# Kernel optimization log

Hardware: AMD Instinct MI355X
Metric: run time of the kernel (lower is better)

The kernel has to match this reference:

```python
import jax, jax.numpy as jnp
import numpy as np

N_HEAD = 16
N_EMBD = 1024
SCALE = 1.0 / np.sqrt(N_EMBD // N_HEAD)
NEG_INF = -1e9


def setup_inputs() -> dict:
    key = jax.random.key(0)
    ks = jax.random.split(key, 9)
    B, T, C = 4, 2048, N_EMBD
    std = 1.0 / np.sqrt(C)
    x = jax.random.normal(ks[0], (B, T, C), dtype=jnp.float32)
    attention_mask = jnp.ones((B, T), dtype=jnp.int32)
    Wq = jax.random.normal(ks[1], (C, C), dtype=jnp.float32) * std
    Wk = jax.random.normal(ks[2], (C, C), dtype=jnp.float32) * std
    Wv = jax.random.normal(ks[3], (C, C), dtype=jnp.float32) * std
    Wp = jax.random.normal(ks[4], (C, C), dtype=jnp.float32) * std
    bq = jax.random.normal(ks[5], (C,), dtype=jnp.float32) * 0.01
    bk = jax.random.normal(ks[6], (C,), dtype=jnp.float32) * 0.01
    bv = jax.random.normal(ks[7], (C,), dtype=jnp.float32) * 0.01
    bp = jax.random.normal(ks[8], (C,), dtype=jnp.float32) * 0.01
    return {"x": x, "attention_mask": attention_mask,
            "Wq": Wq, "bq": bq, "Wk": Wk, "bk": bk,
            "Wv": Wv, "bv": bv, "Wp": Wp, "bp": bp}


def reference(x, attention_mask, Wq, bq, Wk, bk, Wv, bv, Wp, bp):
    B, T, C = x.shape
    H, D = N_HEAD, C // N_HEAD
    # projections -> [B, H, T, D]
    def split_heads(y):
        return y.reshape(B, T, H, D).transpose(0, 2, 1, 3)
    q = split_heads(x @ Wq + bq)
    k = split_heads(x @ Wk + bk)
    v = split_heads(x @ Wv + bv)
    # scores [B, H, T, T]
    att = jnp.einsum('bhqd,bhkd->bhqk', q, k) * SCALE
    causal = jnp.tril(jnp.ones((T, T), dtype=bool))
    att = jnp.where(causal[None, None], att, NEG_INF)
    pad = attention_mask[:, None, None, :] != 0  # [B,1,1,T]
    att = jnp.where(pad, att, NEG_INF)
    att = jax.nn.softmax(att, axis=-1)
    # dropout p=0.0 (eval) -> identity
    y = jnp.einsum('bhqk,bhkd->bhqd', att, v)
    y = y.transpose(0, 2, 1, 3).reshape(B, T, C)
    return y @ Wp + bp
```

## Files before the change

### kernel.cpp

```cpp
#include <hip/hip_runtime.h>

typedef unsigned short u16;
typedef unsigned int u32;
typedef unsigned long long u64;
typedef __bf16 bf16x8 __attribute__((ext_vector_type(8)));
typedef unsigned short u16x8 __attribute__((ext_vector_type(8)));
typedef unsigned short u16x4 __attribute__((ext_vector_type(4)));
typedef unsigned int u32x4 __attribute__((ext_vector_type(4)));
typedef float f32x4 __attribute__((ext_vector_type(4)));

#define B_  4
#define T_  2048
#define C_  1024
#define H_  16
#define D_  64

__device__ __forceinline__ u16 f2b(float f) {
  unsigned u = __builtin_bit_cast(unsigned, f);
  return (u16)((u + 0x8000u) >> 16);
}
__device__ __forceinline__ bf16x8 bcast8(u16x8 v) { return __builtin_bit_cast(bf16x8, v); }

__device__ __forceinline__ void gl_lds16(const void* g, void* l) {
  __builtin_amdgcn_global_load_lds((const __attribute__((address_space(1))) u32*)g,
                                   (__attribute__((address_space(3))) u32*)l, 16, 0, 0);
}

__global__ __launch_bounds__(256) void xconv_kernel(const float* __restrict__ x, u16* __restrict__ xb) {
  const size_t i = ((size_t)blockIdx.x * 256 + threadIdx.x) * 8;
  const float4 a = *reinterpret_cast<const float4*>(x + i);
  const float4 b = *reinterpret_cast<const float4*>(x + i + 4);
  u16x8 h;
  h[0] = f2b(a.x); h[1] = f2b(a.y); h[2] = f2b(a.z); h[3] = f2b(a.w);
  h[4] = f2b(b.x); h[5] = f2b(b.y); h[6] = f2b(b.z); h[7] = f2b(b.w);
  *reinterpret_cast<u16x8*>(xb + i) = h;
}

__global__ void wconv_kernel(const float* __restrict__ Wq, const float* __restrict__ Wk,
                             const float* __restrict__ Wv, const float* __restrict__ Wp,
                             u16* __restrict__ wt) {
  __shared__ float tile[32][33];
  const int z = blockIdx.z;
  const float* W = (z == 0) ? Wq : (z == 1) ? Wk : (z == 2) ? Wv : Wp;
  u16* out = wt + (size_t)z * C_ * C_;
  const int n0 = blockIdx.x * 32, k0 = blockIdx.y * 32;
  const int tx = threadIdx.x, ty = threadIdx.y;
  #pragma unroll
  for (int i = 0; i < 4; ++i)
    tile[ty + i * 8][tx] = W[(size_t)(k0 + ty + i * 8) * C_ + n0 + tx];
  __syncthreads();
  #pragma unroll
  for (int i = 0; i < 4; ++i)
    out[(size_t)(n0 + ty + i * 8) * C_ + k0 + tx] = f2b(tile[tx][ty + i * 8]);
}

#define GSTAGE(ldsbase, gsrc) do {                                                   \
    _Pragma("unroll")                                                                \
    for (int i_ = 0; i_ < 4; ++i_) {                                                 \
      const int off_ = wid * 1024 + i_ * 4096;                                       \
      const int row_ = (off_ >> 7) + (lane >> 3);                                    \
      const int cs_  = ((lane & 7) ^ ((lane >> 3) & 7)) * 16;                        \
      gl_lds16((const char*)(gsrc) + (size_t)row_ * 2048 + cs_,                      \
               (char*)(ldsbase) + off_);                                             \
    }                                                                                \
  } while (0)

__global__ __launch_bounds__(256) void qkv_gemm(const u16* __restrict__ xb,
    const u16* __restrict__ wt, const float* __restrict__ bq,
    const float* __restrict__ bk, const float* __restrict__ bv,
    u16* __restrict__ qkv) {
  __shared__ __attribute__((aligned(16))) u16 As[2][128][64];
  __shared__ __attribute__((aligned(16))) u16 Bs[2][128][64];
  const int id = blockIdx.x;
  const int xcd = id & 7, cc = id >> 3;
  const int bm = xcd * 8 + (cc / 24);
  const int bnt = cc % 24;
  const int tid = threadIdx.x;
  const int lane = tid & 63, wid = tid >> 6;
  const int wr = wid >> 1, wc = wid & 1;
  const int m0 = bm * 128, n0 = bnt * 128;

  f32x4 acc[4][4] = {};

  const char* abase = (const char*)xb + (size_t)m0 * 2048;
  const char* bbase = (const char*)wt + (size_t)n0 * 2048;

  const int ph0 = (((lane >> 4)) ^ (lane & 7)) << 3;
  const int ph1 = ((4 + (lane >> 4)) ^ (lane & 7)) << 3;

  GSTAGE(&As[0][0][0], abase);
  GSTAGE(&Bs[0][0][0], bbase);
  __syncthreads();

  for (int t = 0; t < 16; ++t) {
    const int cur = t & 1;
    if (t + 1 < 16) {
      GSTAGE(&As[cur ^ 1][0][0], abase + (t + 1) * 128);
      GSTAGE(&Bs[cur ^ 1][0][0], bbase + (t + 1) * 128);
    }
    bf16x8 af[2][4], bf[2][4];
    #pragma unroll
    for (int r = 0; r < 4; ++r) {
      const int row = wr * 64 + r * 16 + (lane & 15);
      af[0][r] = bcast8(*reinterpret_cast<const u16x8*>(&As[cur][row][ph0]));
      af[1][r] = bcast8(*reinterpret_cast<const u16x8*>(&As[cur][row][ph1]));
    }
    #pragma unroll
    for (int c = 0; c < 4; ++c) {
      const int row = wc * 64 + c * 16 + (lane & 15);
      bf[0][c] = bcast8(*reinterpret_cast<const u16x8*>(&Bs[cur][row][ph0]));
      bf[1][c] = bcast8(*reinterpret_cast<const u16x8*>(&Bs[cur][row][ph1]));
    }
    #pragma unroll
    for (int kk = 0; kk < 2; ++kk)
      #pragma unroll
      for (int r = 0; r < 4; ++r)
        #pragma unroll
        for (int c = 0; c < 4; ++c)
          acc[r][c] = __builtin_amdgcn_mfma_f32_16x16x32_bf16(af[kk][r], bf[kk][c], acc[r][c], 0, 0, 0);
    __syncthreads();
  }
  const int which = n0 >> 10;
  const float* bias = (which == 0) ? bq : (which == 1) ? bk : bv;
  #pragma unroll
  for (int r = 0; r < 4; ++r) {
    #pragma unroll
    for (int c = 0; c < 4; ++c) {
      const int col = n0 + wc * 64 + c * 16 + (lane & 15);
      const int cold = col & 1023;
      const float bv_ = bias[cold];
      const int h = cold >> 6, d = cold & 63;
      #pragma unroll
      for (int p = 0; p < 4; ++p) {
        const int row = m0 + wr * 64 + r * 16 + (lane >> 4) * 4 + p;
        const int bb = row >> 11, t = row & (T_ - 1);
        int dd = d;
        if (which == 1) dd = (d & 7) | ((((d >> 3) ^ (t & 7)) & 7) << 3);
        qkv[(((size_t)which * 64 + bb * H_ + h) * T_ + t) * D_ + dd] = f2b(acc[r][c][p] + bv_);
      }
    }
  }
}

__global__ __launch_bounds__(256) void vtrans_kernel(const u16* __restrict__ qkv, u16* __restrict__ vt) {
  __shared__ u16 tile[64][64];
  const int bh = blockIdx.y;
  const int t0 = blockIdx.x * 64;
  const u16* V = qkv + (size_t)(128 + bh) * (T_ * D_);
  const int tid = threadIdx.x;
  #pragma unroll
  for (int i = 0; i < 2; ++i) {
    const int tl = (tid >> 3) + i * 32;
    const int d0 = (tid & 7) * 8;
    const u16x8 v = *reinterpret_cast<const u16x8*>(&V[(size_t)(t0 + tl) * D_ + d0]);
    const int swz = (d0 >> 3) << 3;
    #pragma unroll
    for (int j = 0; j < 8; ++j)
      tile[d0 + j][tl ^ swz] = v[j];
  }
  __syncthreads();
  #pragma unroll
  for (int i = 0; i < 2; ++i) {
    const int d = (tid >> 3) + i * 32;
    const int c0 = (tid & 7) * 8;
    const u16x8 w = *reinterpret_cast<const u16x8*>(&tile[d][c0 ^ ((d >> 3) << 3)]);
    const int cc = (((c0 >> 3) ^ (d & 7)) << 3);
    *reinterpret_cast<u16x8*>(&vt[((size_t)bh * D_ + d) * T_ + t0 + cc]) = w;
  }
}

__global__ __launch_bounds__(256) void attn_kernel(const u16* __restrict__ qkv,
    const u16* __restrict__ vt, u16* __restrict__ yb) {
  __shared__ __attribute__((aligned(16))) u16 Ks[2][64][64];
  __shared__ __attribute__((aligned(16))) u16 Vs[2][64][64];
  const int bid = blockIdx.x;
  const int wgid = (bid & 7) * 64 + (bid >> 3);
  const int bh = wgid >> 3, pj = wgid & 7;
  const int tid = threadIdx.x, lane = tid & 63, wid = tid >> 6;
  const int g = lane >> 4;
  const u16* Q  = qkv + (size_t)bh * (T_ * D_);
  const u16* K  = qkv + (size_t)(64 + bh) * (T_ * D_);
  const u16* Vt = vt + (size_t)bh * (D_ * T_);
  const int b_ = bh >> 4, h_ = bh & 15;

  const int sw_off = wid * 2048;
  const int vrow0  = wid * 16 + (lane >> 3);
  const int vcol   = (lane & 7) * 16;

  #pragma unroll 1
  for (int seg = 0; seg < 2; ++seg) {
    const int qt = (seg == 0) ? pj : 15 - pj;
    const int q0 = qt * 128;
    const int nt = 2 * qt + 2;
    const int q0w = q0 + wid * 32;

    bf16x8 qf[2][2];
    #pragma unroll
    for (int r = 0; r < 2; ++r)
      #pragma unroll
      for (int ks = 0; ks < 2; ++ks)
        qf[r][ks] = bcast8(*reinterpret_cast<const u16x8*>(
            &Q[(size_t)(q0 + wid * 32 + r * 16 + (lane & 15)) * D_ + ks * 32 + g * 8]));

    f32x4 o[2][4] = {};
    float l_r[2] = {};

#define STAGE(bufi, tt) do {                                                        \
      const char* ksrc_ = (const char*)(K + (size_t)(tt) * 64 * D_);                \
      const char* vsrc_ = (const char*)(Vt + (size_t)(tt) * 64);                    \
      _Pragma("unroll")                                                             \
      for (int i_ = 0; i_ < 2; ++i_) {                                              \
        const int off_ = sw_off + i_ * 1024;                                        \
        gl_lds16(ksrc_ + off_ + lane * 16, (char*)&Ks[bufi][0][0] + off_);          \
        gl_lds16(vsrc_ + (size_t)(vrow0 + i_ * 8) * (T_ * 2) + vcol,                \
                 (char*)&Vs[bufi][0][0] + off_);                                    \
      }                                                                             \
    } while (0)

    STAGE(0, 0);
    __syncthreads();

    for (int t = 0; t < nt; ++t) {
      const int cur = t & 1;
      if (t + 1 < nt) STAGE((t + 1) & 1, t + 1);
      const int kv0 = t * 64;
      if (kv0 <= q0w + 31) {
        f32x4 s[2][4] = {};
        #pragma unroll
        for (int c = 0; c < 4; ++c) {
          const int krow = c * 16 + (lane & 15);
          const bf16x8 kf0 = bcast8(*reinterpret_cast<const u16x8*>(
              &Ks[cur][krow][(g ^ (krow & 7)) << 3]));
          const bf16x8 kf1 = bcast8(*reinterpret_cast<const u16x8*>(
              &Ks[cur][krow][((g + 4) ^ (krow & 7)) << 3]));
          #pragma unroll
          for (int r = 0; r < 2; ++r) {
            s[r][c] = __builtin_amdgcn_mfma_f32_16x16x32_bf16(kf0, qf[r][0], s[r][c], 0, 0, 0);
            s[r][c] = __builtin_amdgcn_mfma_f32_16x16x32_bf16(kf1, qf[r][1], s[r][c], 0, 0, 0);
          }
        }
        bf16x8 vf[2][4];
        #pragma unroll
        for (int ks = 0; ks < 2; ++ks)
          #pragma unroll
          for (int c = 0; c < 4; ++c) {
            const int drow = c * 16 + (lane & 15);
            const char* rowp = (const char*)&Vs[cur][drow][0];
            const int sb0 = (((4 * ks + (g >> 1)) ^ (drow & 7)) << 4) + (g & 1) * 8;
            const int sb1 = (((4 * ks + 2 + (g >> 1)) ^ (drow & 7)) << 4) + (g & 1) * 8;
            const u64 lo = *reinterpret_cast<const u64*>(rowp + sb0);
            const u64 hi = *reinterpret_cast<const u64*>(rowp + sb1);
            u32x4 vw; vw[0] = (u32)lo; vw[1] = (u32)(lo >> 32); vw[2] = (u32)hi; vw[3] = (u32)(hi >> 32);
            vf[ks][c] = __builtin_bit_cast(bf16x8, vw);
          }
        u32x4 paw[2][2];
#define SMAX(MASKED) do {                                                           \
          _Pragma("unroll")                                                         \
          for (int r = 0; r < 2; ++r) {                                             \
            const int qpos = q0w + r * 16 + (lane & 15);                            \
            _Pragma("unroll")                                                       \
            for (int c = 0; c < 4; ++c) {                                           \
              const int kb = kv0 + c * 16 + g * 4;                                  \
              float e[4];                                                           \
              _Pragma("unroll")                                                     \
              for (int p = 0; p < 4; ++p) {                                         \
                e[p] = exp2f(fmaf(s[r][c][p], 0.1803368801111244f,                  \
                                  -17.312340444387028f));                           \
                if (MASKED) e[p] = (kb + p <= qpos) ? e[p] : 0.0f;                  \
                l_r[r] += e[p];                                                     \
              }                                                                     \
              u32 w0, w1;                                                           \
              asm("v_cvt_pk_bf16_f32 %0, %1, %2" : "=v"(w0) : "v"(e[0]), "v"(e[1]));\
              asm("v_cvt_pk_bf16_f32 %0, %1, %2" : "=v"(w1) : "v"(e[2]), "v"(e[3]));\
              paw[r][c >> 1][(c & 1) * 2] = w0;                                     \
              paw[r][c >> 1][(c & 1) * 2 + 1] = w1;                                 \
            }                                                                       \
          }                                                                         \
        } while (0)
        if (kv0 + 63 <= q0w) SMAX(false); else SMAX(true);
#undef SMAX
        #pragma unroll
        for (int ks = 0; ks < 2; ++ks)
          #pragma unroll
          for (int r = 0; r < 2; ++r) {
            const bf16x8 pa = __builtin_bit_cast(bf16x8, paw[r][ks]);
            #pragma unroll
            for (int c = 0; c < 4; ++c)
              o[r][c] = __builtin_amdgcn_mfma_f32_16x16x32_bf16(pa, vf[ks][c], o[r][c], 0, 0, 0);
          }
      }
      __syncthreads();
    }
#undef STAGE

    #pragma unroll
    for (int r = 0; r < 2; ++r) {
      float l = l_r[r];
      l += __shfl_xor(l, 16);
      l += __shfl_xor(l, 32);
      float linv[4];
      #pragma unroll
      for (int p = 0; p < 4; ++p)
        linv[p] = 1.0f / __shfl(l, g * 4 + p, 64);
      #pragma unroll
      for (int c = 0; c < 4; ++c) {
        const int d = c * 16 + (lane & 15);
        #pragma unroll
        for (int p = 0; p < 4; ++p) {
          const int qrow = q0w + r * 16 + g * 4 + p;
          yb[(size_t)(b_ * T_ + qrow) * C_ + h_ * D_ + d] = f2b(o[r][c][p] * linv[p]);
        }
      }
    }
  }
}

__global__ __launch_bounds__(256) void proj_gemm(const u16* __restrict__ yb,
    const u16* __restrict__ Bt, const float* __restrict__ bias, float* __restrict__ out) {
  __shared__ __attribute__((aligned(16))) u16 As[2][128][64];
  __shared__ __attribute__((aligned(16))) u16 Bs[2][128][64];
  const int id = blockIdx.x;
  const int xcd = id & 7, cc = id >> 3;
  const int bm = xcd * 8 + (cc / 8);
  const int bn = cc % 8;
  const int tid = threadIdx.x;
  const int lane = tid & 63, wid = tid >> 6;
  const int wr = wid >> 1, wc = wid & 1;
  const int m0 = bm * 128, n0 = bn * 128;

  f32x4 acc[4][4] = {};

  const char* abase = (const char*)yb + (size_t)m0 * 2048;
  const char* bbase = (const char*)Bt + (size_t)n0 * 2048;

  const int ph0 = (((lane >> 4)) ^ (lane & 7)) << 3;
  const int ph1 = ((4 + (lane >> 4)) ^ (lane & 7)) << 3;

  GSTAGE(&As[0][0][0], abase);
  GSTAGE(&Bs[0][0][0], bbase);
  __syncthreads();

  for (int t = 0; t < 16; ++t) {
    const int cur = t & 1;
    if (t + 1 < 16) {
      GSTAGE(&As[cur ^ 1][0][0], abase + (t + 1) * 128);
      GSTAGE(&Bs[cur ^ 1][0][0], bbase + (t + 1) * 128);
    }
    bf16x8 af[2][4], bf[2][4];
    #pragma unroll
    for (int r = 0; r < 4; ++r) {
      const int row = wr * 64 + r * 16 + (lane & 15);
      af[0][r] = bcast8(*reinterpret_cast<const u16x8*>(&As[cur][row][ph0]));
      af[1][r] = bcast8(*reinterpret_cast<const u16x8*>(&As[cur][row][ph1]));
    }
    #pragma unroll
    for (int c = 0; c < 4; ++c) {
      const int row = wc * 64 + c * 16 + (lane & 15);
      bf[0][c] = bcast8(*reinterpret_cast<const u16x8*>(&Bs[cur][row][ph0]));
      bf[1][c] = bcast8(*reinterpret_cast<const u16x8*>(&Bs[cur][row][ph1]));
    }
    #pragma unroll
    for (int kk = 0; kk < 2; ++kk)
      #pragma unroll
      for (int r = 0; r < 4; ++r)
        #pragma unroll
        for (int c = 0; c < 4; ++c)
          acc[r][c] = __builtin_amdgcn_mfma_f32_16x16x32_bf16(af[kk][r], bf[kk][c], acc[r][c], 0, 0, 0);
    __syncthreads();
  }
  #pragma unroll
  for (int r = 0; r < 4; ++r)
    #pragma unroll
    for (int c = 0; c < 4; ++c) {
      const int col = n0 + wc * 64 + c * 16 + (lane & 15);
      const float bv_ = bias[col];
      #pragma unroll
      for (int p = 0; p < 4; ++p) {
        const int row = m0 + wr * 64 + r * 16 + (lane >> 4) * 4 + p;
        out[(size_t)row * C_ + col] = acc[r][c][p] + bv_;
      }
    }
}

extern "C" void kernel_launch(void* const* d_in, const int* in_sizes, int n_in,
                              void* d_out, int out_size, void* d_ws, size_t ws_size,
                              hipStream_t stream) {
  (void)in_sizes; (void)n_in; (void)out_size; (void)ws_size;
  const float* x  = (const float*)d_in[0];
  const float* Wq = (const float*)d_in[2];
  const float* bq = (const float*)d_in[3];
  const float* Wk = (const float*)d_in[4];
  const float* bk = (const float*)d_in[5];
  const float* Wv = (const float*)d_in[6];
  const float* bv = (const float*)d_in[7];
  const float* Wp = (const float*)d_in[8];
  const float* bp = (const float*)d_in[9];
  float* out = (float*)d_out;
  char* ws = (char*)d_ws;
  u16* wt  = (u16*)ws;
  u16* qkv = (u16*)(ws + (size_t)8 * 1024 * 1024);
  u16* yb  = (u16*)(ws + (size_t)56 * 1024 * 1024);
  u16* xb  = yb;
  u16* vt  = (u16*)(ws + (size_t)72 * 1024 * 1024);

  xconv_kernel<<<dim3(4096), dim3(256), 0, stream>>>(x, xb);
  wconv_kernel<<<dim3(32, 32, 4), dim3(32, 8), 0, stream>>>(Wq, Wk, Wv, Wp, wt);
  qkv_gemm<<<dim3(1536), dim3(256), 0, stream>>>(xb, wt, bq, bk, bv, qkv);
  vtrans_kernel<<<dim3(32, 64), dim3(256), 0, stream>>>(qkv, vt);
  attn_kernel<<<dim3(512), dim3(256), 0, stream>>>(qkv, vt, yb);
  proj_gemm<<<dim3(512), dim3(256), 0, stream>>>(yb, wt + (size_t)3 * C_ * C_, bp, out);
}
```

Measured before the change: 191.4 us.

## Fuse V transpose into QKV epilogue, deepen attention K/V buffering, MFMA row sums

The QKV GEMM epilogue now writes V directly in the transposed, swizzled layout the attention kernel expects, so the separate vtrans kernel launch and its extra read and write of V go away. The attention kernel moves from double to quadruple LDS buffering and processes two KV tiles per barrier, halving the number of syncthreads. Softmax row sums are now accumulated with an extra MFMA against a ones vector instead of scalar adds and shuffles. This costs more LDS per block, which may lower occupancy, plus an extra MFMA per tile; the row sum is also now taken over bf16-rounded probabilities.

```diff
diff --git a/kernel.cpp b/kernel.cpp
--- a/kernel.cpp
+++ b/kernel.cpp
@@ -68,7 +68,7 @@
 __global__ __launch_bounds__(256) void qkv_gemm(const u16* __restrict__ xb,
     const u16* __restrict__ wt, const float* __restrict__ bq,
     const float* __restrict__ bk, const float* __restrict__ bv,
-    u16* __restrict__ qkv) {
+    u16* __restrict__ qkv, u16* __restrict__ vt) {
   __shared__ __attribute__((aligned(16))) u16 As[2][128][64];
   __shared__ __attribute__((aligned(16))) u16 Bs[2][128][64];
   const int id = blockIdx.x;
@@ -121,58 +121,50 @@
     __syncthreads();
   }
   const int which = n0 >> 10;
-  const float* bias = (which == 0) ? bq : (which == 1) ? bk : bv;
-  #pragma unroll
-  for (int r = 0; r < 4; ++r) {
-    #pragma unroll
-    for (int c = 0; c < 4; ++c) {
-      const int col = n0 + wc * 64 + c * 16 + (lane & 15);
-      const int cold = col & 1023;
-      const float bv_ = bias[cold];
-      const int h = cold >> 6, d = cold & 63;
-      #pragma unroll
-      for (int p = 0; p < 4; ++p) {
-        const int row = m0 + wr * 64 + r * 16 + (lane >> 4) * 4 + p;
-        const int bb = row >> 11, t = row & (T_ - 1);
-        int dd = d;
-        if (which == 1) dd = (d & 7) | ((((d >> 3) ^ (t & 7)) & 7) << 3);
-        qkv[(((size_t)which * 64 + bb * H_ + h) * T_ + t) * D_ + dd] = f2b(acc[r][c][p] + bv_);
+  if (which == 2) {
+    #pragma unroll
+    for (int r = 0; r < 4; ++r) {
+      #pragma unroll
+      for (int c = 0; c < 4; ++c) {
+        const int cold = (n0 + wc * 64 + c * 16 + (lane & 15)) & 1023;
+        const float bv_ = bv[cold];
+        const int h = cold >> 6, d = cold & 63;
+        const int row0 = m0 + wr * 64 + r * 16 + (lane >> 4) * 4;
+        const int bb = row0 >> 11, t0q = row0 & (T_ - 1);
+        const int bh = bb * H_ + h;
+        const u16 w0 = f2b(acc[r][c][0] + bv_), w1 = f2b(acc[r][c][1] + bv_);
+        const u16 w2 = f2b(acc[r][c][2] + bv_), w3 = f2b(acc[r][c][3] + bv_);
+        const u64 wq = (u64)w0 | ((u64)w1 << 16) | ((u64)w2 << 32) | ((u64)w3 << 48);
+        const int tswz = (t0q & ~63) + (((((t0q >> 3) & 7) ^ (d & 7)) << 3)) + (t0q & 7);
+        *reinterpret_cast<u64*>(&vt[((size_t)bh * D_ + d) * T_ + tswz]) = wq;
       }
     }
-  }
-}
-
-__global__ __launch_bounds__(256) void vtrans_kernel(const u16* __restrict__ qkv, u16* __restrict__ vt) {
-  __shared__ u16 tile[64][64];
-  const int bh = blockIdx.y;
-  const int t0 = blockIdx.x * 64;
-  const u16* V = qkv + (size_t)(128 + bh) * (T_ * D_);
-  const int tid = threadIdx.x;
-  #pragma unroll
-  for (int i = 0; i < 2; ++i) {
-    const int tl = (tid >> 3) + i * 32;
-    const int d0 = (tid & 7) * 8;
-    const u16x8 v = *reinterpret_cast<const u16x8*>(&V[(size_t)(t0 + tl) * D_ + d0]);
-    const int swz = (d0 >> 3) << 3;
-    #pragma unroll
-    for (int j = 0; j < 8; ++j)
-      tile[d0 + j][tl ^ swz] = v[j];
-  }
-  __syncthreads();
-  #pragma unroll
-  for (int i = 0; i < 2; ++i) {
-    const int d = (tid >> 3) + i * 32;
-    const int c0 = (tid & 7) * 8;
-    const u16x8 w = *reinterpret_cast<const u16x8*>(&tile[d][c0 ^ ((d >> 3) << 3)]);
-    const int cc = (((c0 >> 3) ^ (d & 7)) << 3);
-    *reinterpret_cast<u16x8*>(&vt[((size_t)bh * D_ + d) * T_ + t0 + cc]) = w;
+  } else {
+    const float* bias = (which == 0) ? bq : bk;
+    #pragma unroll
+    for (int r = 0; r < 4; ++r) {
+      #pragma unroll
+      for (int c = 0; c < 4; ++c) {
+        const int cold = (n0 + wc * 64 + c * 16 + (lane & 15)) & 1023;
+        const float bv_ = bias[cold];
+        const int h = cold >> 6, d = cold & 63;
+        #pragma unroll
+        for (int p = 0; p < 4; ++p) {
+          const int row = m0 + wr * 64 + r * 16 + (lane >> 4) * 4 + p;
+          const int bb = row >> 11, t = row & (T_ - 1);
+          int dd = d;
+          if (which == 1) dd = (d & 7) | ((((d >> 3) ^ (t & 7)) & 7) << 3);
+          qkv[(((size_t)which * 64 + bb * H_ + h) * T_ + t) * D_ + dd] = f2b(acc[r][c][p] + bv_);
+        }
+      }
+    }
   }
 }
 
 __global__ __launch_bounds__(256) void attn_kernel(const u16* __restrict__ qkv,
     const u16* __restrict__ vt, u16* __restrict__ yb) {
-  __shared__ __attribute__((aligned(16))) u16 Ks[2][64][64];
-  __shared__ __attribute__((aligned(16))) u16 Vs[2][64][64];
+  __shared__ __attribute__((aligned(16))) u16 Ks[4][64][64];
+  __shared__ __attribute__((aligned(16))) u16 Vs[4][64][64];
   const int bid = blockIdx.x;
   const int wgid = (bid & 7) * 64 + (bid >> 3);
   const int bh = wgid >> 3, pj = wgid & 7;
@@ -187,6 +179,11 @@
   const int vrow0  = wid * 16 + (lane >> 3);
   const int vcol   = (lane & 7) * 16;
 
+  u16x8 onesw;
+  #pragma unroll
+  for (int j = 0; j < 8; ++j) onesw[j] = 0x3F80;
+  const bf16x8 vones = bcast8(onesw);
+
   #pragma unroll 1
   for (int seg = 0; seg < 2; ++seg) {
     const int qt = (seg == 0) ? pj : 15 - pj;
@@ -203,7 +200,7 @@
             &Q[(size_t)(q0 + wid * 32 + r * 16 + (lane & 15)) * D_ + ks * 32 + g * 8]));
 
     f32x4 o[2][4] = {};
-    float l_r[2] = {};
+    f32x4 o5[2] = {};
 
 #define STAGE(bufi, tt) do {                                                        \
       const char* ksrc_ = (const char*)(K + (size_t)(tt) * 64 * D_);                \
@@ -217,101 +214,99 @@
       }                                                                             \
     } while (0)
 
-    STAGE(0, 0);
-    __syncthreads();
-
-    for (int t = 0; t < nt; ++t) {
-      const int cur = t & 1;
-      if (t + 1 < nt) STAGE((t + 1) & 1, t + 1);
-      const int kv0 = t * 64;
-      if (kv0 <= q0w + 31) {
-        f32x4 s[2][4] = {};
-        #pragma unroll
-        for (int c = 0; c < 4; ++c) {
-          const int krow = c * 16 + (lane & 15);
-          const bf16x8 kf0 = bcast8(*reinterpret_cast<const u16x8*>(
-              &Ks[cur][krow][(g ^ (krow & 7)) << 3]));
-          const bf16x8 kf1 = bcast8(*reinterpret_cast<const u16x8*>(
-              &Ks[cur][krow][((g + 4) ^ (krow & 7)) << 3]));
-          #pragma unroll
-          for (int r = 0; r < 2; ++r) {
-            s[r][c] = __builtin_amdgcn_mfma_f32_16x16x32_bf16(kf0, qf[r][0], s[r][c], 0, 0, 0);
-            s[r][c] = __builtin_amdgcn_mfma_f32_16x16x32_bf16(kf1, qf[r][1], s[r][c], 0, 0, 0);
-          }
-        }
-        bf16x8 vf[2][4];
-        #pragma unroll
-        for (int ks = 0; ks < 2; ++ks)
-          #pragma unroll
-          for (int c = 0; c < 4; ++c) {
-            const int drow = c * 16 + (lane & 15);
-            const char* rowp = (const char*)&Vs[cur][drow][0];
-            const int sb0 = (((4 * ks + (g >> 1)) ^ (drow & 7)) << 4) + (g & 1) * 8;
-            const int sb1 = (((4 * ks + 2 + (g >> 1)) ^ (drow & 7)) << 4) + (g & 1) * 8;
-            const u64 lo = *reinterpret_cast<const u64*>(rowp + sb0);
-            const u64 hi = *reinterpret_cast<const u64*>(rowp + sb1);
-            u32x4 vw; vw[0] = (u32)lo; vw[1] = (u32)(lo >> 32); vw[2] = (u32)hi; vw[3] = (u32)(hi >> 32);
-            vf[ks][c] = __builtin_bit_cast(bf16x8, vw);
-          }
-        u32x4 paw[2][2];
-#define SMAX(MASKED) do {                                                           \
+#define SMAXB(MASKED) do {                                                          \
+      _Pragma("unroll")                                                             \
+      for (int r = 0; r < 2; ++r) {                                                 \
+        const int qpos = q0w + r * 16 + (lane & 15);                                \
+        _Pragma("unroll")                                                           \
+        for (int c = 0; c < 4; ++c) {                                               \
+          const int kb = kv0 + c * 16 + g * 4;                                      \
+          float e[4];                                                               \
           _Pragma("unroll")                                                         \
-          for (int r = 0; r < 2; ++r) {                                             \
-            const int qpos = q0w + r * 16 + (lane & 15);                            \
-            _Pragma("unroll")                                                       \
-            for (int c = 0; c < 4; ++c) {                                           \
-              const int kb = kv0 + c * 16 + g * 4;                                  \
-              float e[4];                                                           \
-              _Pragma("unroll")                                                     \
-              for (int p = 0; p < 4; ++p) {                                         \
-                e[p] = exp2f(fmaf(s[r][c][p], 0.1803368801111244f,                  \
-                                  -17.312340444387028f));                           \
-                if (MASKED) e[p] = (kb + p <= qpos) ? e[p] : 0.0f;                  \
-                l_r[r] += e[p];                                                     \
-              }                                                                     \
-              u32 w0, w1;                                                           \
-              asm("v_cvt_pk_bf16_f32 %0, %1, %2" : "=v"(w0) : "v"(e[0]), "v"(e[1]));\
-              asm("v_cvt_pk_bf16_f32 %0, %1, %2" : "=v"(w1) : "v"(e[2]), "v"(e[3]));\
-              paw[r][c >> 1][(c & 1) * 2] = w0;                                     \
-              paw[r][c >> 1][(c & 1) * 2 + 1] = w1;                                 \
-            }                                                                       \
+          for (int p = 0; p < 4; ++p) {                                             \
+            e[p] = exp2f(fmaf(s[r][c][p], 0.1803368801111244f,                      \
+                              -17.312340444387028f));                               \
+            if (MASKED) e[p] = (kb + p <= qpos) ? e[p] : 0.0f;                      \
           }                                                                         \
-        } while (0)
-        if (kv0 + 63 <= q0w) SMAX(false); else SMAX(true);
-#undef SMAX
-        #pragma unroll
-        for (int ks = 0; ks < 2; ++ks)
-          #pragma unroll
-          for (int r = 0; r < 2; ++r) {
-            const bf16x8 pa = __builtin_bit_cast(bf16x8, paw[r][ks]);
-            #pragma unroll
-            for (int c = 0; c < 4; ++c)
-              o[r][c] = __builtin_amdgcn_mfma_f32_16x16x32_bf16(pa, vf[ks][c], o[r][c], 0, 0, 0);
-          }
-      }
-      __syncthreads();
-    }
-#undef STAGE
-
-    #pragma unroll
-    for (int r = 0; r < 2; ++r) {
-      float l = l_r[r];
-      l += __shfl_xor(l, 16);
-      l += __shfl_xor(l, 32);
-      float linv[4];
-      #pragma unroll
-      for (int p = 0; p < 4; ++p)
-        linv[p] = 1.0f / __shfl(l, g * 4 + p, 64);
+          u32 w0, w1;                                                               \
+          asm("v_cvt_pk_bf16_f32 %0, %1, %2" : "=v"(w0) : "v"(e[0]), "v"(e[1]));    \
+          asm("v_cvt_pk_bf16_f32 %0, %1, %2" : "=v"(w1) : "v"(e[2]), "v"(e[3]));    \
+          paw[r][c >> 1][(c & 1) * 2] = w0;                                         \
+          paw[r][c >> 1][(c & 1) * 2 + 1] = w1;                                     \
+        }                                                                           \
+      }                                                                             \
+    } while (0)
+
+    auto compute = [&](int buf, int tt) {
+      const int kv0 = tt * 64;
+      if (kv0 > q0w + 31) return;
+      f32x4 s[2][4] = {};
       #pragma unroll
       for (int c = 0; c < 4; ++c) {
-        const int d = c * 16 + (lane & 15);
-        #pragma unroll
-        for (int p = 0; p < 4; ++p) {
-          const int qrow = q0w + r * 16 + g * 4 + p;
-          yb[(size_t)(b_ * T_ + qrow) * C_ + h_ * D_ + d] = f2b(o[r][c][p] * linv[p]);
+        const int krow = c * 16 + (lane & 15);
+        const bf16x8 kf0 = bcast8(*reinterpret_cast<const u16x8*>(
+            &Ks[buf][krow][(g ^ (krow & 7)) << 3]));
+        const bf16x8 kf1 = bcast8(*reinterpret_cast<const u16x8*>(
+            &Ks[buf][krow][((g + 4) ^ (krow & 7)) << 3]));
+        #pragma unroll
+        for (int r = 0; r < 2; ++r) {
+          s[r][c] = __builtin_amdgcn_mfma_f32_16x16x32_bf16(kf0, qf[r][0], s[r][c], 0, 0, 0);
+          s[r][c] = __builtin_amdgcn_mfma_f32_16x16x32_bf16(kf1, qf[r][1], s[r][c], 0, 0, 0);
         }
       }
-    }
+      bf16x8 vf[2][4];
+      #pragma unroll
+      for (int ks = 0; ks < 2; ++ks)
+        #pragma unroll
+        for (int c = 0; c < 4; ++c) {
+          const int drow = c * 16 + (lane & 15);
+          const char* rowp = (const char*)&Vs[buf][drow][0];
+          const int sb0 = (((4 * ks + (g >> 1)) ^ (drow & 7)) << 4) + (g & 1) * 8;
+          const int sb1 = (((4 * ks + 2 + (g >> 1)) ^ (drow & 7)) << 4) + (g & 1) * 8;
+          const u64 lo = *reinterpret_cast<const u64*>(rowp + sb0);
+          const u64 hi = *reinterpret_cast<const u64*>(rowp + sb1);
+          u32x4 vw; vw[0] = (u32)lo; vw[1] = (u32)(lo >> 32); vw[2] = (u32)hi; vw[3] = (u32)(hi >> 32);
+          vf[ks][c] = __builtin_bit_cast(bf16x8, vw);
+        }
+      u32x4 paw[2][2];
+      if (kv0 + 63 <= q0w) SMAXB(false); else SMAXB(true);
+      #pragma unroll
+      for (int ks = 0; ks < 2; ++ks)
+        #pragma unroll
+        for (int r = 0; r < 2; ++r) {
+          const bf16x8 pa = __builtin_bit_cast(bf16x8, paw[r][ks]);
+          o5[r] = __builtin_amdgcn_mfma_f32_16x16x32_bf16(pa, vones, o5[r], 0, 0, 0);
+          #pragma unroll
+          for (int c = 0; c < 4; ++c)
+            o[r][c] = __builtin_amdgcn_mfma_f32_16x16x32_bf16(pa, vf[ks][c], o[r][c], 0, 0, 0);
+        }
+    };
+
+    STAGE(0, 0);
+    STAGE(1, 1);
+    __syncthreads();
+
+    for (int t = 0; t < nt; t += 2) {
+      if (t + 2 < nt) { STAGE((t + 2) & 3, t + 2); STAGE((t + 3) & 3, t + 3); }
+      compute(t & 3, t);
+      compute((t + 1) & 3, t + 1);
+      __syncthreads();
+    }
+#undef SMAXB
+#undef STAGE
+
+    #pragma unroll
+    for (int r = 0; r < 2; ++r)
+      #pragma unroll
+      for (int p = 0; p < 4; ++p) {
+        const float linv = 1.0f / o5[r][p];
+        const int qrow = q0w + r * 16 + g * 4 + p;
+        #pragma unroll
+        for (int c = 0; c < 4; ++c) {
+          const int d = c * 16 + (lane & 15);
+          yb[(size_t)(b_ * T_ + qrow) * C_ + h_ * D_ + d] = f2b(o[r][c][p] * linv);
+        }
+      }
   }
 }
 
@@ -405,8 +400,7 @@
 
   xconv_kernel<<<dim3(4096), dim3(256), 0, stream>>>(x, xb);
   wconv_kernel<<<dim3(32, 32, 4), dim3(32, 8), 0, stream>>>(Wq, Wk, Wv, Wp, wt);
-  qkv_gemm<<<dim3(1536), dim3(256), 0, stream>>>(xb, wt, bq, bk, bv, qkv);
-  vtrans_kernel<<<dim3(32, 64), dim3(256), 0, stream>>>(qkv, vt);
+  qkv_gemm<<<dim3(1536), dim3(256), 0, stream>>>(xb, wt, bq, bk, bv, qkv, vt);
   attn_kernel<<<dim3(512), dim3(256), 0, stream>>>(qkv, vt, yb);
   proj_gemm<<<dim3(512), dim3(256), 0, stream>>>(yb, wt + (size_t)3 * C_ * C_, bp, out);
 }
```

New measurement: 185.1 us. -3.3%, faster.
